# Performance work log

Hardware: AMD Instinct MI355X
Metric: run time of the kernel (lower is better)

Reference implementation:

```python
import jax, jax.numpy as jnp
import numpy as np

EMBED_DIM = 1024
NUM_HEADS = 16
HEAD_DIM = EMBED_DIM // NUM_HEADS
MLP_SIZE = 4096
LN_EPS = 1e-5


def setup_inputs() -> dict:
    key = jax.random.key(0)
    ks = jax.random.split(key, 12)
    d, f = EMBED_DIM, MLP_SIZE
    s = lambda fan_in: 1.0 / np.sqrt(fan_in)
    return {
        "x": jax.random.normal(ks[0], (2, 2048, d), dtype=jnp.float32),
        "ln1_g": jnp.ones((d,), jnp.float32),
        "ln1_b": jnp.zeros((d,), jnp.float32),
        "ln2_g": jnp.ones((d,), jnp.float32),
        "ln2_b": jnp.zeros((d,), jnp.float32),
        "w_qkv": jax.random.uniform(ks[1], (d, 3 * d), jnp.float32, -s(d), s(d)),
        "b_qkv": jax.random.uniform(ks[2], (3 * d,), jnp.float32, -s(d), s(d)),
        "w_proj": jax.random.uniform(ks[3], (d, d), jnp.float32, -s(d), s(d)),
        "b_proj": jax.random.uniform(ks[4], (d,), jnp.float32, -s(d), s(d)),
        "w_fc1": jax.random.uniform(ks[5], (d, f), jnp.float32, -s(d), s(d)),
        "b_fc1": jax.random.uniform(ks[6], (f,), jnp.float32, -s(d), s(d)),
        "w_fc2": jax.random.uniform(ks[7], (f, d), jnp.float32, -s(f), s(f)),
        "b_fc2": jax.random.uniform(ks[8], (d,), jnp.float32, -s(f), s(f)),
    }


def _layernorm(x, g, b):
    mu = jnp.mean(x, axis=-1, keepdims=True)
    var = jnp.mean(jnp.square(x - mu), axis=-1, keepdims=True)
    return (x - mu) * jax.lax.rsqrt(var + LN_EPS) * g + b


def reference(x, ln1_g, ln1_b, ln2_g, ln2_b, w_qkv, b_qkv, w_proj, b_proj,
              w_fc1, b_fc1, w_fc2, b_fc2):
    B, N, C = x.shape
    H, D = NUM_HEADS, HEAD_DIM
    scale = D ** -0.5

    # --- attention sub-block (pre-LN) ---
    h = _layernorm(x, ln1_g, ln1_b)
    qkv = h @ w_qkv + b_qkv                      # [B,N,3C]
    qkv = qkv.reshape(B, N, 3, H, D)
    q, k, v = (jnp.moveaxis(qkv, 2, 0)[i].transpose(0, 2, 1, 3) for i in range(3))  # each [B,H,N,D]
    attn = jnp.einsum("bhnd,bhmd->bhnm", q, k) * scale
    attn = jax.nn.softmax(attn, axis=-1)
    o = jnp.einsum("bhnm,bhmd->bhnd", attn, v)   # [B,H,N,D]
    o = o.transpose(0, 2, 1, 3).reshape(B, N, C)
    x = x + (o @ w_proj + b_proj)

    # --- MLP sub-block (pre-LN) ---
    h = _layernorm(x, ln2_g, ln2_b)
    h = jax.nn.gelu(h @ w_fc1 + b_fc1, approximate=False)
    x = x + (h @ w_fc2 + b_fc2)
    return x
```

## Files before the change

kernel.cpp:

```cpp
#include <hip/hip_runtime.h>
#include <hip/hip_bf16.h>

typedef __attribute__((ext_vector_type(8))) __bf16 bf16x8;
typedef __attribute__((ext_vector_type(4))) float f32x4;
typedef unsigned short u16;

__device__ __forceinline__ float bf2f(u16 u) {
    unsigned int i = ((unsigned int)u) << 16;
    return __builtin_bit_cast(float, i);
}
__device__ __forceinline__ u16 f2bf_u16(float f) {
    __hip_bfloat16 h = __float2bfloat16(f);
    return *(u16*)&h;
}
__device__ __forceinline__ float gelu_f(float v) {
    return 0.5f * v * (1.0f + erff(v * 0.70710678118654752440f));
}
__device__ __forceinline__ bool is_f32(const unsigned* p) { return *p == 0x3F800000u; }
__device__ __forceinline__ bf16x8 ld_bf8_b64x2(const u16* p) {
    uint2 lo = *(const uint2*)p;
    uint2 hi = *(const uint2*)(p + 4);
    uint4 v = make_uint4(lo.x, lo.y, hi.x, hi.y);
    return __builtin_bit_cast(bf16x8, v);
}
__device__ __forceinline__ void async16(const void* g, void* l) {
    __builtin_amdgcn_global_load_lds(
        (const __attribute__((address_space(1))) void*)g,
        (__attribute__((address_space(3))) void*)l, 16, 0, 0);
}

__device__ __forceinline__ void conv8(const void* src, u16* dst, long off, bool f32in) {
    if (f32in) {
        const float* s = (const float*)src + off;
        float4 a = *(const float4*)s, b = *(const float4*)(s + 4);
        u16 o[8] = {f2bf_u16(a.x), f2bf_u16(a.y), f2bf_u16(a.z), f2bf_u16(a.w),
                    f2bf_u16(b.x), f2bf_u16(b.y), f2bf_u16(b.z), f2bf_u16(b.w)};
        *(uint4*)(dst + off) = *(const uint4*)o;
    } else {
        *(uint4*)(dst + off) = *(const uint4*)((const u16*)src + off);
    }
}

__global__ __launch_bounds__(256) void conv_bias(
        const void* __restrict__ bq, const void* __restrict__ bp,
        const void* __restrict__ b1, const void* __restrict__ b2,
        u16* dbq, u16* dbp, u16* db1, u16* db2,
        const unsigned* __restrict__ dtp) {
    long e = ((long)blockIdx.x * 256 + threadIdx.x) * 8;
    if (e >= 9216L) return;
    bool f = is_f32(dtp);
    if      (e < 3072L) conv8(bq, dbq, e, f);
    else if (e < 4096L) conv8(bp, dbp, e - 3072L, f);
    else if (e < 8192L) conv8(b1, db1, e - 4096L, f);
    else                conv8(b2, db2, e - 8192L, f);
}

__global__ __launch_bounds__(256) void conv_t(const void* __restrict__ src,
                                              u16* __restrict__ dst,
                                              int K, int N,
                                              const unsigned* __restrict__ dtp) {
    const bool f32in = is_f32(dtp);
    __shared__ u16 T[64 * 68];
    int k0 = blockIdx.y * 64, n0 = blockIdx.x * 64;
    int t = threadIdx.x;
    int kr = t >> 2, nc = (t & 3) * 16;

    u16 tmp[16];
    if (f32in) {
        const float* s = (const float*)src + (size_t)(k0 + kr) * N + n0 + nc;
        float4 a = *(const float4*)s;
        float4 b = *(const float4*)(s + 4);
        float4 c = *(const float4*)(s + 8);
        float4 d = *(const float4*)(s + 12);
        tmp[0]=f2bf_u16(a.x);  tmp[1]=f2bf_u16(a.y);  tmp[2]=f2bf_u16(a.z);  tmp[3]=f2bf_u16(a.w);
        tmp[4]=f2bf_u16(b.x);  tmp[5]=f2bf_u16(b.y);  tmp[6]=f2bf_u16(b.z);  tmp[7]=f2bf_u16(b.w);
        tmp[8]=f2bf_u16(c.x);  tmp[9]=f2bf_u16(c.y);  tmp[10]=f2bf_u16(c.z); tmp[11]=f2bf_u16(c.w);
        tmp[12]=f2bf_u16(d.x); tmp[13]=f2bf_u16(d.y); tmp[14]=f2bf_u16(d.z); tmp[15]=f2bf_u16(d.w);
    } else {
        const u16* s = (const u16*)src + (size_t)(k0 + kr) * N + n0 + nc;
        *(uint4*)&tmp[0] = *(const uint4*)s;
        *(uint4*)&tmp[8] = *(const uint4*)(s + 8);
    }
    u16* dl = &T[kr * 68 + nc];
    #pragma unroll
    for (int j = 0; j < 4; ++j)
        *(uint2*)(dl + 4 * j) = *(const uint2*)&tmp[4 * j];
    __syncthreads();

    int nr = t >> 2, kc = (t & 3) * 16;
    u16 o[16];
    #pragma unroll
    for (int i = 0; i < 16; ++i) o[i] = T[(kc + i) * 68 + nr];
    u16* dp = dst + (size_t)(n0 + nr) * K + k0 + kc;
    *(uint4*)dp       = *(const uint4*)&o[0];
    *(uint4*)(dp + 8) = *(const uint4*)&o[8];
}

__global__ __launch_bounds__(256) void vt_prep(const u16* __restrict__ qkv,
                                               unsigned* __restrict__ vtg) {
    __shared__ unsigned Vt[64 * 32];
    int bx = blockIdx.x;
    int b = bx >> 9, h = (bx >> 5) & 15, kt = bx & 31;
    int t = threadIdx.x;
    int va = t & 31, vdc = t >> 5;
    size_t vb = ((size_t)(b * 2048 + kt * 64 + 2 * va)) * 3072 + 2048 + h * 64 + vdc * 8;
    uint4 v0 = *(const uint4*)(qkv + vb);
    uint4 v1 = *(const uint4*)(qkv + vb + 3072);
    const u16* p0 = (const u16*)&v0;
    const u16* p1 = (const u16*)&v1;
    #pragma unroll
    for (int j = 0; j < 8; ++j)
        Vt[(vdc * 8 + j) * 32 + va] = (unsigned)p0[j] | ((unsigned)p1[j] << 16);
    __syncthreads();
    unsigned* dst = vtg + (size_t)bx * 2048 + t * 8;
    *(uint4*)dst       = *(const uint4*)&Vt[t * 8];
    *(uint4*)(dst + 4) = *(const uint4*)&Vt[t * 8 + 4];
}

__global__ __launch_bounds__(256) void ln_first(const void* __restrict__ xin,
                                                const void* __restrict__ g,
                                                const void* __restrict__ b,
                                                __hip_bfloat16* __restrict__ out,
                                                const unsigned* __restrict__ dtp) {
    const bool f32in = is_f32(dtp);
    int row = blockIdx.x, t = threadIdx.x;
    size_t base = (size_t)row * 1024 + 4 * t;
    float v[4];
    if (f32in) {
        float4 f = *(const float4*)((const float*)xin + base);
        v[0] = f.x; v[1] = f.y; v[2] = f.z; v[3] = f.w;
    } else {
        ushort4 u = *(const ushort4*)((const __hip_bfloat16*)xin + base);
        v[0] = bf2f(u.x); v[1] = bf2f(u.y); v[2] = bf2f(u.z); v[3] = bf2f(u.w);
    }
    float s = v[0] + v[1] + v[2] + v[3];
    float s2 = v[0]*v[0] + v[1]*v[1] + v[2]*v[2] + v[3]*v[3];
    #pragma unroll
    for (int off = 32; off > 0; off >>= 1) {
        s  += __shfl_down(s, off);
        s2 += __shfl_down(s2, off);
    }
    __shared__ float red[8];
    int wave = t >> 6, lane = t & 63;
    if (lane == 0) { red[wave] = s; red[4 + wave] = s2; }
    __syncthreads();
    float S  = red[0] + red[1] + red[2] + red[3];
    float S2 = red[4] + red[5] + red[6] + red[7];
    float mean = S * (1.0f / 1024.0f);
    float var  = S2 * (1.0f / 1024.0f) - mean * mean;
    float rstd = rsqrtf(var + 1e-5f);
    float gg[4], bb[4];
    if (f32in) {
        float4 fg = *(const float4*)((const float*)g + 4 * t);
        float4 fb = *(const float4*)((const float*)b + 4 * t);
        gg[0]=fg.x; gg[1]=fg.y; gg[2]=fg.z; gg[3]=fg.w;
        bb[0]=fb.x; bb[1]=fb.y; bb[2]=fb.z; bb[3]=fb.w;
    } else {
        ushort4 ug = *(const ushort4*)((const __hip_bfloat16*)g + 4 * t);
        ushort4 ub = *(const ushort4*)((const __hip_bfloat16*)b + 4 * t);
        gg[0]=bf2f(ug.x); gg[1]=bf2f(ug.y); gg[2]=bf2f(ug.z); gg[3]=bf2f(ug.w);
        bb[0]=bf2f(ub.x); bb[1]=bf2f(ub.y); bb[2]=bf2f(ub.z); bb[3]=bf2f(ub.w);
    }
    #pragma unroll
    for (int i = 0; i < 4; ++i)
        out[base + i] = __float2bfloat16((v[i] - mean) * rstd * gg[i] + bb[i]);
}

__global__ __launch_bounds__(256) void ln_mid(const float* __restrict__ x,
                                              const void* __restrict__ g,
                                              const void* __restrict__ b,
                                              __hip_bfloat16* __restrict__ out,
                                              const unsigned* __restrict__ dtp) {
    const bool f32in = is_f32(dtp);
    int row = blockIdx.x, t = threadIdx.x;
    size_t base = (size_t)row * 1024 + 4 * t;
    float4 f = *(const float4*)(x + base);
    float v[4] = {f.x, f.y, f.z, f.w};
    float s = v[0] + v[1] + v[2] + v[3];
    float s2 = v[0]*v[0] + v[1]*v[1] + v[2]*v[2] + v[3]*v[3];
    #pragma unroll
    for (int off = 32; off > 0; off >>= 1) {
        s  += __shfl_down(s, off);
        s2 += __shfl_down(s2, off);
    }
    __shared__ float red[8];
    int wave = t >> 6, lane = t & 63;
    if (lane == 0) { red[wave] = s; red[4 + wave] = s2; }
    __syncthreads();
    float S  = red[0] + red[1] + red[2] + red[3];
    float S2 = red[4] + red[5] + red[6] + red[7];
    float mean = S * (1.0f / 1024.0f);
    float var  = S2 * (1.0f / 1024.0f) - mean * mean;
    float rstd = rsqrtf(var + 1e-5f);
    float gg[4], bb[4];
    if (f32in) {
        float4 fg = *(const float4*)((const float*)g + 4 * t);
        float4 fb = *(const float4*)((const float*)b + 4 * t);
        gg[0]=fg.x; gg[1]=fg.y; gg[2]=fg.z; gg[3]=fg.w;
        bb[0]=fb.x; bb[1]=fb.y; bb[2]=fb.z; bb[3]=fb.w;
    } else {
        ushort4 ug = *(const ushort4*)((const __hip_bfloat16*)g + 4 * t);
        ushort4 ub = *(const ushort4*)((const __hip_bfloat16*)b + 4 * t);
        gg[0]=bf2f(ug.x); gg[1]=bf2f(ug.y); gg[2]=bf2f(ug.z); gg[3]=bf2f(ug.w);
        bb[0]=bf2f(ub.x); bb[1]=bf2f(ub.y); bb[2]=bf2f(ub.z); bb[3]=bf2f(ub.w);
    }
    #pragma unroll
    for (int i = 0; i < 4; ++i)
        out[base + i] = __float2bfloat16((v[i] - mean) * rstd * gg[i] + bb[i]);
}

template<int EPI, int BM, int BN, int BK>
__global__ __launch_bounds__(256, 2)
void gemm_bf16(const u16* __restrict__ A,
               const u16* __restrict__ BT,
               const u16* __restrict__ bias,
               const void* __restrict__ res,
               void* __restrict__ outp,
               int M, int N, int K,
               const unsigned* __restrict__ dtp) {
    constexpr int NI = BM / 32, NJ = BN / 32;
    constexpr int ASZ = BM * BK, BSZ = BN * BK;
    constexpr int SMASK = BK / 8 - 1;
    constexpr int SBITS = (BK == 32) ? 2 : 3;
    constexpr int RPA   = 512 / BK;
    constexpr int NASYA = (BM * BK) / 2048;
    constexpr int NASYB = (BN * BK) / 2048;
    const bool f32in = is_f32(dtp);
    __shared__ __align__(16) u16 As[2 * ASZ];
    __shared__ __align__(16) u16 Bs[2 * BSZ];
    (void)M;

    int t = threadIdx.x;
    int w = t >> 6, lane = t & 63;
    int quad = lane >> 4, lq = lane & 15;
    int bm = blockIdx.y * BM, bn = blockIdx.x * BN;
    int wm = (w & 1) * (16 * NI), wn = (w >> 1) * (16 * NJ);

    int sr = lane >> SBITS;
    int scs = ((lane & SMASK) ^ (sr & SMASK)) * 8;
    u16* aldst = &As[w * (BM * BK / 4) + lane * 8];
    const u16* ag = A + (size_t)(bm + w * (BM / 4) + sr) * K + scs;
    u16* bldst = &Bs[w * (BN * BK / 4) + lane * 8];
    const u16* bg = BT + (size_t)(bn + w * (BN / 4) + sr) * K + scs;

    f32x4 acc[NI][NJ];
    #pragma unroll
    for (int i = 0; i < NI; ++i)
        #pragma unroll
        for (int j = 0; j < NJ; ++j)
            #pragma unroll
            for (int r = 0; r < 4; ++r) acc[i][j][r] = 0.0f;

    #pragma unroll
    for (int j = 0; j < NASYA; ++j)
        async16(ag + (size_t)(j * RPA) * K, aldst + j * 512);
    #pragma unroll
    for (int j = 0; j < NASYB; ++j)
        async16(bg + (size_t)(j * RPA) * K, bldst + j * 512);

    const int nIter = K / BK;
    for (int k = 0; k < nIter; ++k) {
        __syncthreads();
        int cur = k & 1;
        if (k + 1 < nIter) {
            int nxt = cur ^ 1;
            const u16* agn = ag + (size_t)(k + 1) * BK;
            #pragma unroll
            for (int j = 0; j < NASYA; ++j)
                async16(agn + (size_t)(j * RPA) * K, aldst + nxt * ASZ + j * 512);
            const u16* bgn = bg + (size_t)(k + 1) * BK;
            #pragma unroll
            for (int j = 0; j < NASYB; ++j)
                async16(bgn + (size_t)(j * RPA) * K, bldst + nxt * BSZ + j * 512);
        }

        const u16* Ac = &As[cur * ASZ];
        const u16* Bc = &Bs[cur * BSZ];
        #pragma unroll
        for (int ks = 0; ks < BK / 32; ++ks) {
            bf16x8 af[NI], bfr[NJ];
            #pragma unroll
            for (int i = 0; i < NI; ++i) {
                int R = wm + 16 * i + lq;
                af[i] = *(const bf16x8*)&Ac[R * BK + ((quad + ks * 4) ^ (R & SMASK)) * 8];
            }
            #pragma unroll
            for (int j = 0; j < NJ; ++j) {
                int R = wn + 16 * j + lq;
                bfr[j] = *(const bf16x8*)&Bc[R * BK + ((quad + ks * 4) ^ (R & SMASK)) * 8];
            }
            #pragma unroll
            for (int i = 0; i < NI; ++i)
                #pragma unroll
                for (int j = 0; j < NJ; ++j)
                    acc[i][j] = __builtin_amdgcn_mfma_f32_16x16x32_bf16(af[i], bfr[j], acc[i][j], 0, 0, 0);
        }
    }

    #pragma unroll
    for (int i = 0; i < NI; ++i) {
        #pragma unroll
        for (int j = 0; j < NJ; ++j) {
            #pragma unroll
            for (int r = 0; r < 4; ++r) {
                int row = bm + wm + 16 * i + quad * 4 + r;
                int col = bn + wn + 16 * j + lq;
                size_t idx = (size_t)row * N + col;
                float v = acc[i][j][r] + bf2f(bias[col]);
                if constexpr (EPI == 0) {
                    ((__hip_bfloat16*)outp)[idx] = __float2bfloat16(v);
                } else if constexpr (EPI == 1) {
                    v += f32in ? ((const float*)res)[idx]
                               : bf2f(((const u16*)res)[idx]);
                    ((float*)outp)[idx] = v;
                } else if constexpr (EPI == 2) {
                    ((__hip_bfloat16*)outp)[idx] = __float2bfloat16(gelu_f(v));
                } else {
                    v += ((const float*)res)[idx];
                    if (f32in) ((float*)outp)[idx] = v;
                    else       ((__hip_bfloat16*)outp)[idx] = __float2bfloat16(v);
                }
            }
        }
    }
}

__global__ __launch_bounds__(256, 4)
void attn_mfma(const __hip_bfloat16* __restrict__ qkv,
               const unsigned* __restrict__ vtg,
               __hip_bfloat16* __restrict__ o_out) {
    __shared__ __align__(16) u16 Ks[64 * 72];
    __shared__ __align__(16) unsigned Vt[64 * 36];
    __shared__ __align__(16) u16 Ps[64 * 68];

    int t = threadIdx.x;
    int lane = t & 63, w = t >> 6;
    int quad = lane >> 4, lq = lane & 15;
    int bx = blockIdx.x;
    int b  = bx >> 9, h = (bx >> 5) & 15, qt = bx & 31;
    size_t tok0 = (size_t)b * 2048;

    {
        int key = t >> 2, ld = (t & 3) * 16;
        size_t qb = (tok0 + (size_t)qt * 64 + key) * 3072 + h * 64 + ld;
        uint4 a0 = *(const uint4*)(qkv + qb);
        uint4 a1 = *(const uint4*)(qkv + qb + 8);
        const u16* s0 = (const u16*)&a0;
        const u16* s1 = (const u16*)&a1;
        u16 q16[16];
        #pragma unroll
        for (int j = 0; j < 8; ++j) {
            q16[j]     = f2bf_u16(bf2f(s0[j]) * 0.125f);
            q16[8 + j] = f2bf_u16(bf2f(s1[j]) * 0.125f);
        }
        u16* dst = &Ps[key * 68 + ld];
        #pragma unroll
        for (int j4 = 0; j4 < 4; ++j4)
            *(uint2*)(dst + 4 * j4) = *(const uint2*)&q16[4 * j4];
    }
    __syncthreads();
    bf16x8 qf0 = ld_bf8_b64x2(&Ps[(w * 16 + lq) * 68 + quad * 8]);
    bf16x8 qf1 = ld_bf8_b64x2(&Ps[(w * 16 + lq) * 68 + quad * 8 + 32]);

    f32x4 oacc[4];
    #pragma unroll
    for (int dt = 0; dt < 4; ++dt)
        #pragma unroll
        for (int r = 0; r < 4; ++r) oacc[dt][r] = 0.0f;
    float m_run = -1e30f, l_run = 0.0f;

    int skey = t >> 2, sld = (t & 3) * 16;
    int vrow = t >> 2, vcol = (t & 3) * 8;

    uint4 k0, k1, w0, w1;
    {
        size_t kb = (tok0 + (size_t)skey) * 3072 + 1024 + h * 64 + sld;
        k0 = *(const uint4*)(qkv + kb);
        k1 = *(const uint4*)(qkv + kb + 8);
        const unsigned* vg = vtg + ((size_t)(b * 512 + h * 32)) * 2048 + t * 8;
        w0 = *(const uint4*)vg;
        w1 = *(const uint4*)(vg + 4);
    }

    for (int kt = 0; kt < 32; ++kt) {
        __syncthreads();
        *(uint4*)&Ks[skey * 72 + sld]     = k0;
        *(uint4*)&Ks[skey * 72 + sld + 8] = k1;
        unsigned* vdst = &Vt[vrow * 36 + vcol];
        *(uint4*)vdst       = w0;
        *(uint4*)(vdst + 4) = w1;
        __syncthreads();
        if (kt + 1 < 32) {
            size_t kb = (tok0 + (size_t)(kt + 1) * 64 + skey) * 3072 + 1024 + h * 64 + sld;
            k0 = *(const uint4*)(qkv + kb);
            k1 = *(const uint4*)(qkv + kb + 8);
            const unsigned* vg = vtg + ((size_t)(b * 512 + h * 32 + kt + 1)) * 2048 + t * 8;
            w0 = *(const uint4*)vg;
            w1 = *(const uint4*)(vg + 4);
        }

        f32x4 sacc[4];
        #pragma unroll
        for (int j = 0; j < 4; ++j)
            #pragma unroll
            for (int r = 0; r < 4; ++r) sacc[j][r] = 0.0f;
        __builtin_amdgcn_s_setprio(1);
        #pragma unroll
        for (int j = 0; j < 4; ++j) {
            const u16* kr = &Ks[(j * 16 + lq) * 72 + quad * 8];
            bf16x8 kf0 = *(const bf16x8*)kr;
            bf16x8 kf1 = *(const bf16x8*)(kr + 32);
            sacc[j] = __builtin_amdgcn_mfma_f32_16x16x32_bf16(kf0, qf0, sacc[j], 0, 0, 0);
            sacc[j] = __builtin_amdgcn_mfma_f32_16x16x32_bf16(kf1, qf1, sacc[j], 0, 0, 0);
        }
        __builtin_amdgcn_s_setprio(0);

        float mx = sacc[0][0];
        #pragma unroll
        for (int j = 0; j < 4; ++j)
            #pragma unroll
            for (int r = 0; r < 4; ++r) mx = fmaxf(mx, sacc[j][r]);
        mx = fmaxf(mx, __shfl_xor(mx, 16));
        mx = fmaxf(mx, __shfl_xor(mx, 32));
        if (!__all(mx <= m_run + 8.0f)) {
            float mnew = fmaxf(m_run, mx);
            float alpha = __expf(m_run - mnew);
            l_run *= alpha;
            #pragma unroll
            for (int dt = 0; dt < 4; ++dt)
                #pragma unroll
                for (int r = 0; r < 4; ++r) oacc[dt][r] *= alpha;
            m_run = mnew;
        }

        float ls = 0.0f;
        int prow = (w * 16 + lq) * 68;
        #pragma unroll
        for (int j = 0; j < 4; ++j) {
            float p0 = __expf(sacc[j][0] - m_run);
            float p1 = __expf(sacc[j][1] - m_run);
            float p2 = __expf(sacc[j][2] - m_run);
            float p3 = __expf(sacc[j][3] - m_run);
            ls += (p0 + p1) + (p2 + p3);
            u16 pk[4] = {f2bf_u16(p0), f2bf_u16(p1), f2bf_u16(p2), f2bf_u16(p3)};
            *(uint2*)&Ps[prow + quad * 4 + 16 * j] = *(const uint2*)pk;
        }
        ls += __shfl_xor(ls, 16);
        ls += __shfl_xor(ls, 32);
        l_run += ls;

        bf16x8 pf0 = ld_bf8_b64x2(&Ps[prow + quad * 8]);
        bf16x8 pf1 = ld_bf8_b64x2(&Ps[prow + quad * 8 + 32]);
        __builtin_amdgcn_s_setprio(1);
        #pragma unroll
        for (int dt = 0; dt < 4; ++dt) {
            const unsigned* vr = &Vt[(dt * 16 + lq) * 36 + quad * 4];
            bf16x8 vf0 = __builtin_bit_cast(bf16x8, *(const uint4*)vr);
            bf16x8 vf1 = __builtin_bit_cast(bf16x8, *(const uint4*)(vr + 16));
            oacc[dt] = __builtin_amdgcn_mfma_f32_16x16x32_bf16(vf0, pf0, oacc[dt], 0, 0, 0);
            oacc[dt] = __builtin_amdgcn_mfma_f32_16x16x32_bf16(vf1, pf1, oacc[dt], 0, 0, 0);
        }
        __builtin_amdgcn_s_setprio(0);
    }

    __syncthreads();
    u16* T = Ks;
    float inv = 1.0f / l_run;
    int trow = (w * 16 + lq) * 68;
    #pragma unroll
    for (int dt = 0; dt < 4; ++dt) {
        u16 pk[4] = {f2bf_u16(oacc[dt][0] * inv), f2bf_u16(oacc[dt][1] * inv),
                     f2bf_u16(oacc[dt][2] * inv), f2bf_u16(oacc[dt][3] * inv)};
        *(uint2*)&T[trow + quad * 4 + 16 * dt] = *(const uint2*)pk;
    }
    __syncthreads();
    {
        int q = t >> 2, dc = (t & 3) * 16;
        const u16* src = &T[q * 68 + dc];
        uint2 a0 = *(const uint2*)src;
        uint2 a1 = *(const uint2*)(src + 4);
        uint2 a2 = *(const uint2*)(src + 8);
        uint2 a3 = *(const uint2*)(src + 12);
        u16* op = (u16*)o_out + (tok0 + (size_t)qt * 64 + q) * 1024 + h * 64 + dc;
        *(uint4*)op       = make_uint4(a0.x, a0.y, a1.x, a1.y);
        *(uint4*)(op + 8) = make_uint4(a2.x, a2.y, a3.x, a3.y);
    }
}

extern "C" void kernel_launch(void* const* d_in, const int* in_sizes, int n_in,
                              void* d_out, int out_size, void* d_ws, size_t ws_size,
                              hipStream_t stream) {
    (void)in_sizes; (void)n_in; (void)out_size; (void)ws_size;
    const void* x      = d_in[0];
    const void* ln1_g  = d_in[1];
    const void* ln1_b  = d_in[2];
    const void* ln2_g  = d_in[3];
    const void* ln2_b  = d_in[4];
    const void* w_qkv  = d_in[5];
    const void* b_qkv  = d_in[6];
    const void* w_proj = d_in[7];
    const void* b_proj = d_in[8];
    const void* w_fc1  = d_in[9];
    const void* b_fc1  = d_in[10];
    const void* w_fc2  = d_in[11];
    const void* b_fc2  = d_in[12];
    const unsigned* probe = (const unsigned*)ln1_g;

    constexpr int Mtok = 4096;
    char* ws = (char*)d_ws;
    __hip_bfloat16* bufA = (__hip_bfloat16*)ws;
    __hip_bfloat16* qkvb = (__hip_bfloat16*)(ws + ((size_t)8 << 20));
    float*          x1   = (float*)(ws + ((size_t)8 << 20));
    u16*            w1T  = (u16*)(ws + ((size_t)24 << 20));
    u16*            wqT  = (u16*)(ws + ((size_t)32 << 20));
    u16*            wpT  = (u16*)(ws + ((size_t)38 << 20));
    unsigned*       vtg  = (unsigned*)(ws + ((size_t)40 << 20));
    __hip_bfloat16* g1   = (__hip_bfloat16*)(ws + ((size_t)32 << 20));
    u16*            w2T  = (u16*)ws;
    char* BZ = ws + ((size_t)64 << 20);
    u16* bqb = (u16*)BZ;
    u16* bpb = (u16*)(BZ + 8192);
    u16* b1b = (u16*)(BZ + 16384);
    u16* b2b = (u16*)(BZ + 24576);

    conv_bias<<<5, 256, 0, stream>>>(b_qkv, b_proj, b_fc1, b_fc2,
                                     bqb, bpb, b1b, b2b, probe);
    conv_t<<<dim3(3072 / 64, 1024 / 64), 256, 0, stream>>>(w_qkv, wqT, 1024, 3072, probe);
    conv_t<<<dim3(1024 / 64, 1024 / 64), 256, 0, stream>>>(w_proj, wpT, 1024, 1024, probe);
    ln_first<<<Mtok, 256, 0, stream>>>(x, ln1_g, ln1_b, bufA, probe);
    gemm_bf16<0, 128, 128, 32><<<dim3(3072 / 128, Mtok / 128), 256, 0, stream>>>(
        (const u16*)bufA, wqT, bqb, nullptr, qkvb, Mtok, 3072, 1024, probe);
    vt_prep<<<1024, 256, 0, stream>>>((const u16*)qkvb, vtg);
    attn_mfma<<<1024, 256, 0, stream>>>(qkvb, vtg, bufA);
    conv_t<<<dim3(4096 / 64, 1024 / 64), 256, 0, stream>>>(w_fc1, w1T, 1024, 4096, probe);
    gemm_bf16<1, 64, 64, 64><<<dim3(1024 / 64, Mtok / 64), 256, 0, stream>>>(
        (const u16*)bufA, wpT, bpb, x, x1, Mtok, 1024, 1024, probe);
    ln_mid<<<Mtok, 256, 0, stream>>>(x1, ln2_g, ln2_b, bufA, probe);
    gemm_bf16<2, 128, 128, 32><<<dim3(4096 / 128, Mtok / 128), 256, 0, stream>>>(
        (const u16*)bufA, w1T, b1b, nullptr, g1, Mtok, 4096, 1024, probe);
    conv_t<<<dim3(1024 / 64, 4096 / 64), 256, 0, stream>>>(w_fc2, w2T, 4096, 1024, probe);
    gemm_bf16<3, 64, 64, 64><<<dim3(1024 / 64, Mtok / 64), 256, 0, stream>>>(
        (const u16*)g1, w2T, b2b, x1, d_out, Mtok, 1024, 4096, probe);
}
```

Baseline: 372.7 us.

## Double-buffer attention K/V tiles via async LDS loads with XOR swizzle

```diff
diff --git a/kernel.cpp b/kernel.cpp
--- a/kernel.cpp
+++ b/kernel.cpp
@@ -17,12 +17,6 @@
     return 0.5f * v * (1.0f + erff(v * 0.70710678118654752440f));
 }
 __device__ __forceinline__ bool is_f32(const unsigned* p) { return *p == 0x3F800000u; }
-__device__ __forceinline__ bf16x8 ld_bf8_b64x2(const u16* p) {
-    uint2 lo = *(const uint2*)p;
-    uint2 hi = *(const uint2*)(p + 4);
-    uint4 v = make_uint4(lo.x, lo.y, hi.x, hi.y);
-    return __builtin_bit_cast(bf16x8, v);
-}
 __device__ __forceinline__ void async16(const void* g, void* l) {
     __builtin_amdgcn_global_load_lds(
         (const __attribute__((address_space(1))) void*)g,
@@ -112,9 +106,11 @@
     for (int j = 0; j < 8; ++j)
         Vt[(vdc * 8 + j) * 32 + va] = (unsigned)p0[j] | ((unsigned)p1[j] << 16);
     __syncthreads();
-    unsigned* dst = vtg + (size_t)bx * 2048 + t * 8;
-    *(uint4*)dst       = *(const uint4*)&Vt[t * 8];
-    *(uint4*)(dst + 4) = *(const uint4*)&Vt[t * 8 + 4];
+    int R = t >> 2, u = t & 3;
+    unsigned* dst = vtg + (size_t)bx * 2048 + R * 32;
+    const unsigned* src = &Vt[R * 32 + u * 8];
+    *(uint4*)(dst + (((2 * u)     ^ (R & 7)) * 4)) = *(const uint4*)src;
+    *(uint4*)(dst + (((2 * u + 1) ^ (R & 7)) * 4)) = *(const uint4*)(src + 4);
 }
 
 __global__ __launch_bounds__(256) void ln_first(const void* __restrict__ xin,
@@ -329,16 +325,29 @@
 void attn_mfma(const __hip_bfloat16* __restrict__ qkv,
                const unsigned* __restrict__ vtg,
                __hip_bfloat16* __restrict__ o_out) {
-    __shared__ __align__(16) u16 Ks[64 * 72];
-    __shared__ __align__(16) unsigned Vt[64 * 36];
-    __shared__ __align__(16) u16 Ps[64 * 68];
+    __shared__ __align__(16) u16      Ks[2][64 * 64];
+    __shared__ __align__(16) unsigned Vt[2][64 * 32];
+    __shared__ __align__(16) u16      Ps[64 * 64];
 
     int t = threadIdx.x;
     int lane = t & 63, w = t >> 6;
     int quad = lane >> 4, lq = lane & 15;
-    int bx = blockIdx.x;
+    int bxh = blockIdx.x;
+    int bx  = (bxh & 7) * 128 + (bxh >> 3);
     int b  = bx >> 9, h = (bx >> 5) & 15, qt = bx & 31;
     size_t tok0 = (size_t)b * 2048;
+
+    int srow  = w * 16 + (lane >> 3);
+    int kslot = ((lane & 7) ^ (lane >> 3)) * 8;
+    const u16* kg = (const u16*)qkv + (tok0 + srow) * 3072 + 1024 + h * 64 + kslot;
+    const unsigned* vg = vtg + ((size_t)(b * 512 + h * 32)) * 2048 + w * 512 + lane * 4;
+    u16*      kd = &Ks[0][0] + w * 1024 + lane * 8;
+    unsigned* vd = &Vt[0][0] + w * 512  + lane * 4;
+
+    async16(kg, kd);
+    async16(kg + (size_t)8 * 3072, kd + 512);
+    async16(vg, vd);
+    async16(vg + 256, vd + 256);
 
     {
         int key = t >> 2, ld = (t & 3) * 16;
@@ -353,52 +362,44 @@
             q16[j]     = f2bf_u16(bf2f(s0[j]) * 0.125f);
             q16[8 + j] = f2bf_u16(bf2f(s1[j]) * 0.125f);
         }
-        u16* dst = &Ps[key * 68 + ld];
-        #pragma unroll
-        for (int j4 = 0; j4 < 4; ++j4)
-            *(uint2*)(dst + 4 * j4) = *(const uint2*)&q16[4 * j4];
-    }
-    __syncthreads();
-    bf16x8 qf0 = ld_bf8_b64x2(&Ps[(w * 16 + lq) * 68 + quad * 8]);
-    bf16x8 qf1 = ld_bf8_b64x2(&Ps[(w * 16 + lq) * 68 + quad * 8 + 32]);
+        int k7 = key & 7;
+        #pragma unroll
+        for (int j4 = 0; j4 < 4; ++j4) {
+            int c = ld + 4 * j4;
+            *(uint2*)&Ps[key * 64 + (((c >> 3) ^ k7) * 8) + (c & 7)] =
+                *(const uint2*)&q16[4 * j4];
+        }
+    }
+    __syncthreads();
+
+    int x7 = lq & 7;
+    int Rq = w * 16 + lq;
+    bf16x8 qf0 = *(const bf16x8*)&Ps[Rq * 64 + ((quad ^ x7) * 8)];
+    bf16x8 qf1 = *(const bf16x8*)&Ps[Rq * 64 + (((4 + quad) ^ x7) * 8)];
 
     f32x4 oacc[4];
     #pragma unroll
     for (int dt = 0; dt < 4; ++dt)
         #pragma unroll
         for (int r = 0; r < 4; ++r) oacc[dt][r] = 0.0f;
+    const float L2E = 1.44269504f;
     float m_run = -1e30f, l_run = 0.0f;
-
-    int skey = t >> 2, sld = (t & 3) * 16;
-    int vrow = t >> 2, vcol = (t & 3) * 8;
-
-    uint4 k0, k1, w0, w1;
-    {
-        size_t kb = (tok0 + (size_t)skey) * 3072 + 1024 + h * 64 + sld;
-        k0 = *(const uint4*)(qkv + kb);
-        k1 = *(const uint4*)(qkv + kb + 8);
-        const unsigned* vg = vtg + ((size_t)(b * 512 + h * 32)) * 2048 + t * 8;
-        w0 = *(const uint4*)vg;
-        w1 = *(const uint4*)(vg + 4);
-    }
+    float m2 = m_run * L2E;
 
     for (int kt = 0; kt < 32; ++kt) {
-        __syncthreads();
-        *(uint4*)&Ks[skey * 72 + sld]     = k0;
-        *(uint4*)&Ks[skey * 72 + sld + 8] = k1;
-        unsigned* vdst = &Vt[vrow * 36 + vcol];
-        *(uint4*)vdst       = w0;
-        *(uint4*)(vdst + 4) = w1;
-        __syncthreads();
+        int cur = kt & 1;
+        if (kt) __syncthreads();
         if (kt + 1 < 32) {
-            size_t kb = (tok0 + (size_t)(kt + 1) * 64 + skey) * 3072 + 1024 + h * 64 + sld;
-            k0 = *(const uint4*)(qkv + kb);
-            k1 = *(const uint4*)(qkv + kb + 8);
-            const unsigned* vg = vtg + ((size_t)(b * 512 + h * 32 + kt + 1)) * 2048 + t * 8;
-            w0 = *(const uint4*)vg;
-            w1 = *(const uint4*)(vg + 4);
-        }
-
+            int nxt = cur ^ 1;
+            const u16* kn = kg + (size_t)(kt + 1) * 64 * 3072;
+            async16(kn, kd + nxt * 4096);
+            async16(kn + (size_t)8 * 3072, kd + nxt * 4096 + 512);
+            const unsigned* vn = vg + (size_t)(kt + 1) * 2048;
+            async16(vn, vd + nxt * 2048);
+            async16(vn + 256, vd + nxt * 2048 + 256);
+        }
+
+        const u16* KC = &Ks[0][0] + cur * 4096;
         f32x4 sacc[4];
         #pragma unroll
         for (int j = 0; j < 4; ++j)
@@ -407,9 +408,9 @@
         __builtin_amdgcn_s_setprio(1);
         #pragma unroll
         for (int j = 0; j < 4; ++j) {
-            const u16* kr = &Ks[(j * 16 + lq) * 72 + quad * 8];
-            bf16x8 kf0 = *(const bf16x8*)kr;
-            bf16x8 kf1 = *(const bf16x8*)(kr + 32);
+            int R = j * 16 + lq;
+            bf16x8 kf0 = *(const bf16x8*)&KC[R * 64 + ((quad ^ x7) * 8)];
+            bf16x8 kf1 = *(const bf16x8*)&KC[R * 64 + (((4 + quad) ^ x7) * 8)];
             sacc[j] = __builtin_amdgcn_mfma_f32_16x16x32_bf16(kf0, qf0, sacc[j], 0, 0, 0);
             sacc[j] = __builtin_amdgcn_mfma_f32_16x16x32_bf16(kf1, qf1, sacc[j], 0, 0, 0);
         }
@@ -424,39 +425,42 @@
         mx = fmaxf(mx, __shfl_xor(mx, 32));
         if (!__all(mx <= m_run + 8.0f)) {
             float mnew = fmaxf(m_run, mx);
-            float alpha = __expf(m_run - mnew);
+            float alpha = exp2f((m_run - mnew) * L2E);
             l_run *= alpha;
             #pragma unroll
             for (int dt = 0; dt < 4; ++dt)
                 #pragma unroll
                 for (int r = 0; r < 4; ++r) oacc[dt][r] *= alpha;
             m_run = mnew;
+            m2 = m_run * L2E;
         }
 
         float ls = 0.0f;
-        int prow = (w * 16 + lq) * 68;
+        int prow = Rq * 64;
         #pragma unroll
         for (int j = 0; j < 4; ++j) {
-            float p0 = __expf(sacc[j][0] - m_run);
-            float p1 = __expf(sacc[j][1] - m_run);
-            float p2 = __expf(sacc[j][2] - m_run);
-            float p3 = __expf(sacc[j][3] - m_run);
+            float p0 = exp2f(__builtin_fmaf(sacc[j][0], L2E, -m2));
+            float p1 = exp2f(__builtin_fmaf(sacc[j][1], L2E, -m2));
+            float p2 = exp2f(__builtin_fmaf(sacc[j][2], L2E, -m2));
+            float p3 = exp2f(__builtin_fmaf(sacc[j][3], L2E, -m2));
             ls += (p0 + p1) + (p2 + p3);
             u16 pk[4] = {f2bf_u16(p0), f2bf_u16(p1), f2bf_u16(p2), f2bf_u16(p3)};
-            *(uint2*)&Ps[prow + quad * 4 + 16 * j] = *(const uint2*)pk;
+            int c = quad * 4 + 16 * j;
+            *(uint2*)&Ps[prow + (((c >> 3) ^ x7) * 8) + (c & 7)] = *(const uint2*)pk;
         }
         ls += __shfl_xor(ls, 16);
         ls += __shfl_xor(ls, 32);
         l_run += ls;
 
-        bf16x8 pf0 = ld_bf8_b64x2(&Ps[prow + quad * 8]);
-        bf16x8 pf1 = ld_bf8_b64x2(&Ps[prow + quad * 8 + 32]);
+        bf16x8 pf0 = *(const bf16x8*)&Ps[prow + ((quad ^ x7) * 8)];
+        bf16x8 pf1 = *(const bf16x8*)&Ps[prow + (((4 + quad) ^ x7) * 8)];
+        const unsigned* VC = &Vt[0][0] + cur * 2048;
         __builtin_amdgcn_s_setprio(1);
         #pragma unroll
         for (int dt = 0; dt < 4; ++dt) {
-            const unsigned* vr = &Vt[(dt * 16 + lq) * 36 + quad * 4];
-            bf16x8 vf0 = __builtin_bit_cast(bf16x8, *(const uint4*)vr);
-            bf16x8 vf1 = __builtin_bit_cast(bf16x8, *(const uint4*)(vr + 16));
+            int R = dt * 16 + lq;
+            bf16x8 vf0 = __builtin_bit_cast(bf16x8, *(const uint4*)&VC[R * 32 + ((quad ^ x7) * 4)]);
+            bf16x8 vf1 = __builtin_bit_cast(bf16x8, *(const uint4*)&VC[R * 32 + (((4 + quad) ^ x7) * 4)]);
             oacc[dt] = __builtin_amdgcn_mfma_f32_16x16x32_bf16(vf0, pf0, oacc[dt], 0, 0, 0);
             oacc[dt] = __builtin_amdgcn_mfma_f32_16x16x32_bf16(vf1, pf1, oacc[dt], 0, 0, 0);
         }
@@ -464,7 +468,7 @@
     }
 
     __syncthreads();
-    u16* T = Ks;
+    u16* T = &Ks[0][0];
     float inv = 1.0f / l_run;
     int trow = (w * 16 + lq) * 68;
     #pragma unroll
```

Measured after the change: 380.3 us. 1.02x slower.
